# Optimization experiments

Hardware: AMD Instinct MI355X
Metric: run time of the kernel (lower is better)

The kernel has to match this reference:

```python
import jax, jax.numpy as jnp
import numpy as np

STRIDE = 4
NUM_HEADS = 8


def _make_window(x, stride, nh):
    # (B,C,H,W) -> (B, nh, S, S, (H/S)*(W/S), C/nh)
    b, c, h, w = x.shape
    x = x.reshape(b, nh, c // nh, h // stride, stride, w // stride, stride)
    x = x.transpose(0, 1, 4, 6, 3, 5, 2)
    return x.reshape(b, nh, stride, stride, (h // stride) * (w // stride), c // nh)


def _demake_window(x, h, w):
    # (B, nh, S, S, L, dh) -> (B, nh*dh, H, W)
    b, nh, s, _, L, dh = x.shape
    x = x.reshape(b, nh, s, s, h // s, w // s, dh)
    x = x.transpose(0, 1, 6, 4, 2, 5, 3)
    return x.reshape(b, nh * dh, h, w)


def _proj(x, W, bias):
    # 1x1 conv == per-pixel GEMM: (B,C,H,W),(O,C) -> (B,O,H,W)
    return jnp.einsum('bchw,oc->bohw', x, W) + bias[None, :, None, None]


def setup_inputs() -> dict:
    key = jax.random.key(0)
    ks = jax.random.split(key, 12)
    B, C, H, W = 4, 256, 64, 64
    P, V, O = 256, 256, 256  # proj/value/out channels
    inp = {
        'fea_q': jax.random.normal(ks[0], (B, C, H, W), jnp.float32),
        'fea_k': jax.random.normal(ks[1], (B, C, H, W), jnp.float32),
        'fea_v': jax.random.normal(ks[2], (B, V, H, W), jnp.float32),
        'mask_q': (jax.random.uniform(ks[3], (B, 1, H, W)) > 0.5).astype(jnp.float32),
        'mask_k': (jax.random.uniform(ks[4], (B, 1, H, W)) > 0.5).astype(jnp.float32),
        'q_w': jax.random.normal(ks[5], (P, C), jnp.float32) * 0.02,
        'q_b': jnp.zeros((P,), jnp.float32),
        'k_w': jax.random.normal(ks[6], (P, C), jnp.float32) * 0.02,
        'k_b': jnp.zeros((P,), jnp.float32),
        'v_w': jax.random.normal(ks[7], (O, V), jnp.float32) * 0.02,
        'v_b': jnp.zeros((O,), jnp.float32),
    }
    return inp


def reference(fea_q, fea_k, fea_v, mask_q, mask_k, q_w, q_b, k_w, k_b, v_w, v_b):
    B, _, H, W = fea_q.shape
    head_dim = q_w.shape[0] // NUM_HEADS
    scaling = head_dim ** (-0.5)

    query = _make_window(_proj(fea_q, q_w, q_b), STRIDE, NUM_HEADS)
    key = _make_window(_proj(fea_k, k_w, k_b), STRIDE, NUM_HEADS)
    value = _make_window(_proj(fea_v, v_w, v_b), STRIDE, NUM_HEADS)

    # (B, nh, S, S, L, L)
    weights = jnp.matmul(query, jnp.swapaxes(key, -1, -2)) * scaling

    # mask attention (no-grad in original)
    mq = _make_window(jax.lax.stop_gradient(mask_q), STRIDE, 1)
    mk = _make_window(jax.lax.stop_gradient(mask_k), STRIDE, 1)
    mask_attn = jnp.matmul(mq, jnp.swapaxes(mk, -1, -2))  # (B,1,S,S,L,L)
    mask_sum = jnp.sum(mask_attn, axis=-1, keepdims=True)
    mask_attn = mask_attn + (mask_sum == 0).astype(jnp.float32)
    mask_attn = jnp.where(mask_attn == 0, -jnp.inf,
                          jnp.where(mask_attn == 1, 0.0, mask_attn))
    weights = weights + mask_attn

    weights = jax.nn.softmax(weights, axis=-1)  # dropout p=0 -> identity
    weights = weights * (1.0 - (mask_sum == 0).astype(jnp.float32))

    out = jnp.matmul(weights, value)  # (B, nh, S, S, L, dh)
    return _demake_window(out, H, W)
```

## Files before the change

### kernel.cpp

```cpp
#include <hip/hip_runtime.h>
#include <hip/hip_bf16.h>

#define NH 8
#define DH 32
#define LW 256
#define HW 4096
#define CIN 256

typedef float f32x4 __attribute__((ext_vector_type(4)));
typedef short s16x8 __attribute__((ext_vector_type(8)));
typedef short s16x4 __attribute__((ext_vector_type(4)));

#define AS1 __attribute__((address_space(1)))
#define AS3 __attribute__((address_space(3)))

__device__ __forceinline__ short f2bf(float f) {
  __hip_bfloat16 h = __float2bfloat16(f);
  short s; __builtin_memcpy(&s, &h, 2); return s;
}

__device__ __forceinline__ void gload_lds16(const void* g, void* l) {
  __builtin_amdgcn_global_load_lds((const AS1 void*)g, (AS3 void*)l, 16, 0, 0);
}

#define KOFF 4194304
#define VOFF 8388608
#define WTOFF 12582912

__global__ void wconv_kernel(const float* __restrict__ qw, const float* __restrict__ kw,
                             const float* __restrict__ vw, short* __restrict__ ws) {
  int blk = blockIdx.x;
  int t = blk >> 5, kb = blk & 31;
  const float* W = (t == 0) ? qw : ((t == 1) ? kw : vw);
  int o = threadIdx.x;
  f32x4 w0 = *(const f32x4*)(W + o * CIN + kb * 8);
  f32x4 w1 = *(const f32x4*)(W + o * CIN + kb * 8 + 4);
  s16x8 v;
#pragma unroll
  for (int j = 0; j < 4; ++j) { v[j] = f2bf(w0[j]); v[4 + j] = f2bf(w1[j]); }
  *(s16x8*)(ws + WTOFF + (blk * 256 + o) * 8) = v;
}

__global__ void __launch_bounds__(256, 3)
proj_kernel(const float* __restrict__ fq, const float* __restrict__ fk,
            const float* __restrict__ fv,
            const float* __restrict__ qb, const float* __restrict__ kb_,
            const float* __restrict__ vb,
            short* __restrict__ ws) {
  __shared__ s16x8 SMEM[2048];

  int bid = blockIdx.x;
  int orig = (bid & 7) * 96 + (bid >> 3);
  int t = orig >> 8;
  int r0 = orig & 255;
  int b = r0 >> 6;
  int pblk = (r0 >> 1) & 31;
  int oblk = r0 & 1;

  const float* fea = (t == 0) ? fq : ((t == 1) ? fk : fv);
  const float* Bv  = (t == 0) ? qb : ((t == 1) ? kb_ : vb);
  const short* Wt  = ws + WTOFF + t * 65536;

  int p0 = pblk * 128, o0 = oblk * 128;
  int tid = threadIdx.x;
  int lane = tid & 63, wv = tid >> 6;
  int g = lane >> 4, li = lane & 15;

  const f32x4 fzero = {0.f, 0.f, 0.f, 0.f};
  f32x4 acc[2][8];
#pragma unroll
  for (int m = 0; m < 2; ++m)
#pragma unroll
    for (int n = 0; n < 8; ++n) acc[m][n] = fzero;

  const float* feab = fea + b * (CIN * HW);
  int coct = tid >> 5;
  int pq = (tid & 31) * 4;

  f32x4 ldB[8];

#define LOAD_B(cs_) do { int c0_ = (cs_) * 64; _Pragma("unroll") \
  for (int j_ = 0; j_ < 8; ++j_) \
    ldB[j_] = *(const f32x4*)(feab + (c0_ + coct * 8 + j_) * HW + p0 + pq); } while (0)

#define WRITE_B(buf_) do { _Pragma("unroll") \
  for (int pp_ = 0; pp_ < 4; ++pp_) { s16x8 v_; _Pragma("unroll") \
    for (int j_ = 0; j_ < 8; ++j_) v_[j_] = f2bf(ldB[j_][pp_]); \
    int p_ = pq + pp_; int pidx_ = p_ ^ ((p_ >> 3) & 7); \
    SMEM[(buf_) * 1024 + coct * 128 + pidx_] = v_; } } while (0)

  LOAD_B(0);
  WRITE_B(0);
  __syncthreads();

  for (int cs = 0; cs < 4; ++cs) {
    if (cs < 3) LOAD_B(cs + 1);
#pragma unroll
    for (int kk = 0; kk < 2; ++kk) {
      int kbg = cs * 8 + kk * 4 + g;
      const short* abase = Wt + (kbg * 256 + o0 + wv * 32 + li) * 8;
      s16x8 a0 = *(const s16x8*)(abase);
      s16x8 a1 = *(const s16x8*)(abase + 128);
#pragma unroll
      for (int n = 0; n < 8; ++n) {
        int p = n * 16 + li;
        int pidx = p ^ ((p >> 3) & 7);
        s16x8 bb = SMEM[(cs & 1) * 1024 + (kk * 4 + g) * 128 + pidx];
        acc[0][n] = __builtin_amdgcn_mfma_f32_16x16x32_bf16(a0, bb, acc[0][n], 0, 0, 0);
        acc[1][n] = __builtin_amdgcn_mfma_f32_16x16x32_bf16(a1, bb, acc[1][n], 0, 0, 0);
      }
    }
    if (cs < 3) {
      WRITE_B((cs + 1) & 1);
      __syncthreads();
    }
  }
#undef LOAD_B
#undef WRITE_B

  float bias_r[2][4];
#pragma unroll
  for (int m = 0; m < 2; ++m)
#pragma unroll
    for (int rr = 0; rr < 4; ++rr)
      bias_r[m][rr] = Bv[o0 + wv * 32 + m * 16 + g * 4 + rr];

  if (t != 2) {
    int nh = oblk * 4 + wv;
#pragma unroll
    for (int m = 0; m < 2; ++m) {
      int kb = m * 2 + (g >> 1);
      int dlo = (g & 1) * 4;
#pragma unroll
      for (int n = 0; n < 8; ++n) {
        int p = p0 + n * 16 + li;
        int h = p >> 6, w = p & 63;
        int s1 = h & 3, h0 = h >> 2, s2 = w & 3, w0 = w >> 2;
        int wwin = s1 * 4 + s2, l = h0 * 16 + w0;
        int winbase = (b * NH + nh) * 16 + wwin;
        s16x4 v;
#pragma unroll
        for (int rr = 0; rr < 4; ++rr) v[rr] = f2bf(acc[m][n][rr] + bias_r[m][rr]);
        short* dst = ws + (t == 0 ? 0 : KOFF);
        *(s16x4*)(dst + winbase * 8192 + (kb * 256 + l) * 8 + dlo) = v;
      }
    }
  } else {
    __syncthreads();
    short* Tr = (short*)SMEM;
#pragma unroll
    for (int m = 0; m < 2; ++m) {
      int ob = wv * 32 + m * 16 + g * 4;
#pragma unroll
      for (int n = 0; n < 8; ++n) {
        int p = n * 16 + li;
        s16x4 v;
#pragma unroll
        for (int rr = 0; rr < 4; ++rr) v[rr] = f2bf(acc[m][n][rr] + bias_r[m][rr]);
        *(s16x4*)(Tr + p * 128 + (ob ^ ((p & 15) << 2))) = v;
      }
    }
    __syncthreads();
    int d128 = tid >> 1;
    int h_idx = tid & 1;
    int nh2 = (o0 + d128) >> 5, d = (o0 + d128) & 31;
    int hh = (p0 >> 6) + h_idx;
    int s1e = hh & 3, h0e = hh >> 2;
#pragma unroll
    for (int j = 0; j < 8; ++j) {
      int s2e = j & 3, woct = j >> 2;
      s16x8 v;
#pragma unroll
      for (int k = 0; k < 8; ++k) {
        int pl = h_idx * 64 + s2e + 32 * woct + 4 * k;
        v[k] = Tr[pl * 128 + (d128 ^ ((pl & 15) << 2))];
      }
      int wwin = s1e * 4 + s2e;
      int l_oct = h0e * 2 + woct;
      int winbase = (b * NH + nh2) * 16 + wwin;
      *(s16x8*)(ws + VOFF + winbase * 8192 + d * 256 + l_oct * 8) = v;
    }
  }
}

__global__ void __launch_bounds__(256, 4)
attn_kernel(const short* __restrict__ ws, const float* __restrict__ mq,
            const float* __restrict__ mk, float* __restrict__ out) {
  __shared__ s16x8 KsV[1024];
  __shared__ s16x8 PsV[512];
  __shared__ float amaskS[256];
  __shared__ float mqS[128];
  __shared__ float facS[128];
  __shared__ int anyS[4];

  int bid = blockIdx.x;
  int orig = (bid & 7) * 128 + (bid >> 3);
  int qh = orig & 1;
  int s2 = (orig >> 1) & 3, s1 = (orig >> 3) & 3, nh = (orig >> 5) & 7, b = orig >> 8;
  int wwin = s1 * 4 + s2;
  int tid = threadIdx.x;
  int lane = tid & 63, wv = tid >> 6, g = lane >> 4, li = lane & 15;

  int winbase = (b * NH + nh) * 16 + wwin;
  const short* qt = ws + winbase * 8192;
  const short* kt = ws + KOFF + winbase * 8192;
  const short* vt = ws + VOFF + winbase * 8192;

#pragma unroll
  for (int i = 0; i < 4; ++i) {
    int seg = i * 4 + wv;
    gload_lds16(kt + (seg * 64 + lane) * 8, &KsV[seg * 64]);
  }

  {
    int l = tid;
    int h = (l >> 4) * 4 + s1, w = (l & 15) * 4 + s2;
    float mkv = mk[b * HW + h * 64 + w];
    amaskS[l] = (mkv > 0.5f) ? 0.0f : -1e30f;
    unsigned long long bal = __ballot(mkv > 0.5f);
    if (lane == 0) anyS[wv] = (bal != 0ULL) ? 1 : 0;
  }
  if (tid < 128) {
    int l = qh * 128 + tid;
    int h = (l >> 4) * 4 + s1, w = (l & 15) * 4 + s2;
    mqS[tid] = mq[b * HW + h * 64 + w];
  }

  int lq0 = wv * 32;
  s16x8 qa[2];
#pragma unroll
  for (int m = 0; m < 2; ++m)
    qa[m] = *(const s16x8*)(qt + (g * 256 + qh * 128 + lq0 + m * 16 + li) * 8);

  __syncthreads();
  int anyk = anyS[0] | anyS[1] | anyS[2] | anyS[3];

  const f32x4 fzero = {0.f, 0.f, 0.f, 0.f};
  f32x4 of[2][2];
#pragma unroll
  for (int m = 0; m < 2; ++m) { of[m][0] = fzero; of[m][1] = fzero; }
  float rs[8];
#pragma unroll
  for (int i = 0; i < 8; ++i) rs[i] = 0.0f;

  const float C = 0.17677669529663689f * 1.4426950408889634f;

#pragma unroll
  for (int lkb = 0; lkb < 4; ++lkb) {
    f32x4 sa[2][4];
#pragma unroll
    for (int n = 0; n < 4; ++n) {
      s16x8 kf = KsV[g * 256 + lkb * 64 + n * 16 + li];
#pragma unroll
      for (int m = 0; m < 2; ++m)
        sa[m][n] = __builtin_amdgcn_mfma_f32_16x16x32_bf16(qa[m], kf, fzero, 0, 0, 0);
    }
#pragma unroll
    for (int ks = 0; ks < 2; ++ks) {
#pragma unroll
      for (int n2 = 0; n2 < 2; ++n2) {
        int n = ks * 2 + n2;
        float am = amaskS[lkb * 64 + n * 16 + li];
#pragma unroll
        for (int m = 0; m < 2; ++m) {
#pragma unroll
          for (int rr = 0; rr < 4; ++rr) {
            float pval = exp2f(sa[m][n][rr] * C + am);
            rs[m * 4 + rr] += pval;
            int row = m * 16 + g * 4 + rr;
            int cl = n * 16 + li;
            int kbh = (cl >> 3) & 3;
            short* ps = (short*)&PsV[wv * 128 + kbh * 32 + row];
            ps[cl & 7] = f2bf(pval);
          }
        }
      }
      int kg = lkb * 2 + ks;
      s16x8 pb[2];
#pragma unroll
      for (int n = 0; n < 2; ++n) pb[n] = PsV[wv * 128 + g * 32 + n * 16 + li];
#pragma unroll
      for (int m2 = 0; m2 < 2; ++m2) {
        s16x8 va = *(const s16x8*)(vt + (m2 * 16 + li) * 256 + (kg * 4 + g) * 8);
#pragma unroll
        for (int n = 0; n < 2; ++n)
          of[m2][n] = __builtin_amdgcn_mfma_f32_16x16x32_bf16(va, pb[n], of[m2][n], 0, 0, 0);
      }
    }
  }

#pragma unroll
  for (int i = 0; i < 8; ++i) {
    float v = rs[i];
    v += __shfl_xor(v, 1);
    v += __shfl_xor(v, 2);
    v += __shfl_xor(v, 4);
    v += __shfl_xor(v, 8);
    rs[i] = v;
  }
  if (li == 0) {
#pragma unroll
    for (int m = 0; m < 2; ++m)
#pragma unroll
      for (int rr = 0; rr < 4; ++rr) {
        int row = m * 16 + g * 4 + rr;
        float sum = rs[m * 4 + rr];
        facS[wv * 32 + row] = (anyk && mqS[wv * 32 + row] > 0.5f) ? (1.0f / sum) : 0.0f;
      }
  }

#pragma unroll
  for (int m2 = 0; m2 < 2; ++m2) {
#pragma unroll
    for (int n = 0; n < 2; ++n) {
      int lloc = wv * 32 + n * 16;
      float fac = facS[lloc + li];
      int l = qh * 128 + lloc;
      int h = (l >> 4) * 4 + s1;
      int w = li * 4 + s2;
#pragma unroll
      for (int rr = 0; rr < 4; ++rr) {
        int o = nh * 32 + m2 * 16 + g * 4 + rr;
        out[((b * 256 + o) * 64 + h) * 64 + w] = of[m2][n][rr] * fac;
      }
    }
  }
}

extern "C" void kernel_launch(void* const* d_in, const int* in_sizes, int n_in,
                              void* d_out, int out_size, void* d_ws, size_t ws_size,
                              hipStream_t stream) {
  const float* fq = (const float*)d_in[0];
  const float* fk = (const float*)d_in[1];
  const float* fv = (const float*)d_in[2];
  const float* mq = (const float*)d_in[3];
  const float* mk = (const float*)d_in[4];
  const float* qw = (const float*)d_in[5];
  const float* qb = (const float*)d_in[6];
  const float* kw = (const float*)d_in[7];
  const float* kb = (const float*)d_in[8];
  const float* vw = (const float*)d_in[9];
  const float* vb = (const float*)d_in[10];
  short* ws = (short*)d_ws;

  wconv_kernel<<<96, 256, 0, stream>>>(qw, kw, vw, ws);
  proj_kernel<<<768, 256, 0, stream>>>(fq, fk, fv, qb, kb, vb, ws);
  attn_kernel<<<1024, 256, 0, stream>>>(ws, mq, mk, (float*)d_out);
}
```

Before: 51.92 us.

## Stage Q/K projection output through LDS for 16-byte stores; retile V layout

The projection kernel now stages all outputs (Q, K and V) through a padded LDS transpose buffer (row stride 136) instead of using an XOR swizzle. Q and K are then written with 16-byte vector stores instead of scattered 8-byte stores. The V layout in the workspace is retiled so each 16-byte chunk holds 8 consecutive positions for one channel, and the attention kernel's V load index is changed to match, giving more contiguous accesses. The main cp loop is also fully unrolled. This adds an LDS round trip and a barrier for Q/K, and LDS use grows slightly, which may lower occupancy.

```diff
diff --git a/kernel.cpp b/kernel.cpp
--- a/kernel.cpp
+++ b/kernel.cpp
@@ -47,7 +47,7 @@
             const float* __restrict__ qb, const float* __restrict__ kb_,
             const float* __restrict__ vb,
             short* __restrict__ ws) {
-  __shared__ s16x8 SMEM[2048];
+  __shared__ s16x8 SMEM[2304];
 
   int bid = blockIdx.x;
   int orig = (bid & 7) * 96 + (bid >> 3);
@@ -93,6 +93,7 @@
   WRITE_B(0);
   __syncthreads();
 
+#pragma unroll
   for (int cs = 0; cs < 4; ++cs) {
     if (cs < 3) LOAD_B(cs + 1);
 #pragma unroll
@@ -125,45 +126,44 @@
     for (int rr = 0; rr < 4; ++rr)
       bias_r[m][rr] = Bv[o0 + wv * 32 + m * 16 + g * 4 + rr];
 
+  __syncthreads();
+  short* Tr = (short*)SMEM;
+#pragma unroll
+  for (int m = 0; m < 2; ++m) {
+    int ob = wv * 32 + m * 16 + g * 4;
+#pragma unroll
+    for (int n = 0; n < 8; ++n) {
+      int p = n * 16 + li;
+      s16x4 v;
+#pragma unroll
+      for (int rr = 0; rr < 4; ++rr) v[rr] = f2bf(acc[m][n][rr] + bias_r[m][rr]);
+      *(s16x4*)(Tr + p * 136 + ob) = v;
+    }
+  }
+  __syncthreads();
+
   if (t != 2) {
-    int nh = oblk * 4 + wv;
-#pragma unroll
-    for (int m = 0; m < 2; ++m) {
-      int kb = m * 2 + (g >> 1);
-      int dlo = (g & 1) * 4;
-#pragma unroll
-      for (int n = 0; n < 8; ++n) {
-        int p = p0 + n * 16 + li;
-        int h = p >> 6, w = p & 63;
-        int s1 = h & 3, h0 = h >> 2, s2 = w & 3, w0 = w >> 2;
-        int wwin = s1 * 4 + s2, l = h0 * 16 + w0;
-        int winbase = (b * NH + nh) * 16 + wwin;
-        s16x4 v;
-#pragma unroll
-        for (int rr = 0; rr < 4; ++rr) v[rr] = f2bf(acc[m][n][rr] + bias_r[m][rr]);
-        short* dst = ws + (t == 0 ? 0 : KOFF);
-        *(s16x4*)(dst + winbase * 8192 + (kb * 256 + l) * 8 + dlo) = v;
-      }
+    short* dst = ws + (t == 0 ? 0 : KOFF);
+#pragma unroll
+    for (int it = 0; it < 8; ++it) {
+      int c = it * 256 + tid;
+      int o8 = (c >> 7) << 3;
+      int pl = c & 127;
+      s16x8 v = *(const s16x8*)(Tr + pl * 136 + o8);
+      int pg = p0 + pl;
+      int h = pg >> 6, w = pg & 63;
+      int s1 = h & 3, h0 = h >> 2, s2 = w & 3, w0 = w >> 2;
+      int wwin = s1 * 4 + s2, l = h0 * 16 + w0;
+      int o = o0 + o8;
+      int nh = o >> 5, kb = (o & 31) >> 3;
+      int winbase = (b * NH + nh) * 16 + wwin;
+      *(s16x8*)(dst + winbase * 8192 + (kb * 256 + l) * 8) = v;
     }
   } else {
-    __syncthreads();
-    short* Tr = (short*)SMEM;
-#pragma unroll
-    for (int m = 0; m < 2; ++m) {
-      int ob = wv * 32 + m * 16 + g * 4;
-#pragma unroll
-      for (int n = 0; n < 8; ++n) {
-        int p = n * 16 + li;
-        s16x4 v;
-#pragma unroll
-        for (int rr = 0; rr < 4; ++rr) v[rr] = f2bf(acc[m][n][rr] + bias_r[m][rr]);
-        *(s16x4*)(Tr + p * 128 + (ob ^ ((p & 15) << 2))) = v;
-      }
-    }
-    __syncthreads();
     int d128 = tid >> 1;
     int h_idx = tid & 1;
-    int nh2 = (o0 + d128) >> 5, d = (o0 + d128) & 31;
+    int o = o0 + d128;
+    int nh2 = o >> 5, d = o & 31;
     int hh = (p0 >> 6) + h_idx;
     int s1e = hh & 3, h0e = hh >> 2;
 #pragma unroll
@@ -173,12 +173,13 @@
 #pragma unroll
       for (int k = 0; k < 8; ++k) {
         int pl = h_idx * 64 + s2e + 32 * woct + 4 * k;
-        v[k] = Tr[pl * 128 + (d128 ^ ((pl & 15) << 2))];
+        v[k] = Tr[pl * 136 + d128];
       }
       int wwin = s1e * 4 + s2e;
       int l_oct = h0e * 2 + woct;
       int winbase = (b * NH + nh2) * 16 + wwin;
-      *(s16x8*)(ws + VOFF + winbase * 8192 + d * 256 + l_oct * 8) = v;
+      int idx = (l_oct >> 2) * 1024 + (l_oct & 3) * 256 + (d >> 4) * 128 + (d & 15) * 8;
+      *(s16x8*)(ws + VOFF + winbase * 8192 + idx) = v;
     }
   }
 }
@@ -281,7 +282,7 @@
       for (int n = 0; n < 2; ++n) pb[n] = PsV[wv * 128 + g * 32 + n * 16 + li];
 #pragma unroll
       for (int m2 = 0; m2 < 2; ++m2) {
-        s16x8 va = *(const s16x8*)(vt + (m2 * 16 + li) * 256 + (kg * 4 + g) * 8);
+        s16x8 va = *(const s16x8*)(vt + (kg * 4 + g) * 256 + m2 * 128 + li * 8);
 #pragma unroll
         for (int n = 0; n < 2; ++n)
           of[m2][n] = __builtin_amdgcn_mfma_f32_16x16x32_bf16(va, pb[n], of[m2][n], 0, 0, 0);
```

Result: faster. 48.60 us (-6.4%).
